# Kernel optimization log

Measured on AMD Instinct MI355X. Metric: run time of the kernel, lower is better.

The kernel has to match this reference:

```python
import jax, jax.numpy as jnp
import numpy as np

B, M, Q, D = 32, 8192, 64, 128

def setup_inputs() -> dict:
    key = jax.random.key(0)
    k1, k2, k3, k4 = jax.random.split(key, 4)
    story_a = jax.random.normal(k1, (B, M, D), dtype=jnp.float32)
    u = jax.random.normal(k2, (B, Q, D), dtype=jnp.float32)
    story_c = jax.random.normal(k3, (B, M, D), dtype=jnp.float32)
    H = jax.random.normal(k4, (D, D), dtype=jnp.float32) * (1.0 / np.sqrt(D))
    return {"story_a": story_a, "u": u, "story_c": story_c, "H": H}

def reference(story_a, u, story_c, H):
    # scores: Dot(axes=-1)([story_a, u]) -> (B, M, Q)
    m = jnp.einsum('bmd,bqd->bmq', story_a, u)
    # Keras Softmax() default axis=-1: normalize over Q (faithful to original)
    p = jax.nn.softmax(m, axis=-1)          # (B, M, Q)
    p = jnp.swapaxes(p, 1, 2)                # (B, Q, M)
    # output memory: Dot(axes=(2,1))([p, story_c]) -> (B, Q, D)
    c = jnp.einsum('bqm,bmd->bqd', p, story_c)
    # linear residual: K.dot(u, H) + c
    mapped_u = jnp.einsum('bqd,de->bqe', u, H)
    return c + mapped_u
```

## Files before the change

### kernel.cpp

```cpp
#include <hip/hip_runtime.h>

#define B_ 32
#define M_ 8192
#define Q_ 64
#define D_ 128
#define MT 64
#define LDA 136
#define LDP 72

typedef __attribute__((ext_vector_type(8))) short short8;
typedef __attribute__((ext_vector_type(4))) float floatx4;

__device__ __forceinline__ unsigned pkbf(float a, float b) {
  unsigned ua = __builtin_bit_cast(unsigned, a) + 0x8000u;
  unsigned ub = __builtin_bit_cast(unsigned, b) + 0x8000u;
  return __builtin_amdgcn_perm(ub, ua, 0x07060302u);
}

template <int CTRL>
__device__ __forceinline__ float dppadd(float x) {
  int y = __builtin_amdgcn_update_dpp(0, __builtin_bit_cast(int, x), CTRL, 0xF, 0xF, true);
  return x + __builtin_bit_cast(float, y);
}
__device__ __forceinline__ float rowsum16(float x) {
  x = dppadd<0x128>(x); x = dppadd<0x124>(x);
  x = dppadd<0x122>(x); x = dppadd<0x121>(x);
  return x;
}

__device__ __forceinline__ void barrier_lds() {
  asm volatile("s_waitcnt lgkmcnt(0)\n\ts_barrier" ::: "memory");
}

__global__ __launch_bounds__(256) void pack_u(const float* __restrict__ U,
                                              short8* __restrict__ ufrag) {
  int t = blockIdx.x * 256 + threadIdx.x;
  int lane = t & 63, ks = (t >> 6) & 3, qs = (t >> 8) & 3, b = t >> 10;
  int l15 = lane & 15, quad = (lane >> 4) & 3;
  const float* p = U + ((size_t)b * Q_ + 16 * qs + l15) * D_ + 32 * ks + 8 * quad;
  float4 x = *(const float4*)p;
  float4 y = *(const float4*)(p + 4);
  union { unsigned u[4]; short8 v; } o;
  o.u[0] = pkbf(x.x, x.y); o.u[1] = pkbf(x.z, x.w);
  o.u[2] = pkbf(y.x, y.y); o.u[3] = pkbf(y.z, y.w);
  ufrag[t] = o.v;
}

__global__ __launch_bounds__(256, 4) void memn2n_main(
    const float* __restrict__ A, const float* __restrict__ Cc,
    const short8* __restrict__ ufrag, float* __restrict__ dst,
    int chunks, int use_atomic) {
  __shared__ __align__(16) unsigned short sAP[MT * LDA];
  __shared__ __align__(16) unsigned short sC[MT * LDA];
  unsigned short* const sA = sAP;
  unsigned short* const sP = sAP;

  const int tid  = threadIdx.x;
  const int lane = tid & 63;
  const int w    = tid >> 6;
  const int l15  = lane & 15;
  const int quad = (lane >> 4) & 3;

  const int blk = blockIdx.x;
  const int b   = blk / chunks;
  const int ch  = blk - b * chunks;
  const int Mc  = M_ / chunks;
  const int nT  = Mc / MT;

  const int g = tid & 31;
  const int r = tid >> 5;

  const short8* ufb = ufrag + (size_t)b * 16 * 64 + lane;

  floatx4 acc[2][4];
#pragma unroll
  for (int i = 0; i < 2; ++i)
#pragma unroll
    for (int j = 0; j < 4; ++j) acc[i][j] = (floatx4){0.f, 0.f, 0.f, 0.f};

  const float* Abase = A + ((size_t)b * M_ + (size_t)ch * Mc) * D_;
  const float* Cbase = Cc + ((size_t)b * M_ + (size_t)ch * Mc) * D_;

  for (int t = 0; t < nT; ++t) {
    const float* At = Abase + (size_t)t * MT * D_;
    const float* Ct = Cbase + (size_t)t * MT * D_;
    barrier_lds();
#pragma unroll
    for (int i = 0; i < 8; ++i) {
      int mi = r + 8 * i;
      float4 v = *(const float4*)(At + mi * D_ + 4 * g);
      *(uint2*)&sA[mi * LDA + 4 * g] = make_uint2(pkbf(v.x, v.y), pkbf(v.z, v.w));
    }
#pragma unroll
    for (int i = 0; i < 8; ++i) {
      int mi = r + 8 * i;
      float4 v = *(const float4*)(Ct + mi * D_ + 4 * g);
      *(uint2*)&sC[mi * LDA + 4 * g] = make_uint2(pkbf(v.x, v.y), pkbf(v.z, v.w));
    }
    barrier_lds();

    floatx4 s1[4];
#pragma unroll
    for (int qs = 0; qs < 4; ++qs) s1[qs] = (floatx4){0.f, 0.f, 0.f, 0.f};
#pragma unroll
    for (int ks = 0; ks < 4; ++ks) {
      short8 af = *(const short8*)&sA[(16 * w + l15) * LDA + 32 * ks + 8 * quad];
#pragma unroll
      for (int qs = 0; qs < 4; ++qs) {
        short8 bfv = ufb[(qs * 4 + ks) * 64];
        s1[qs] = __builtin_amdgcn_mfma_f32_16x16x32_bf16(af, bfv, s1[qs], 0, 0, 0);
      }
    }
    barrier_lds();

    float pv[4][4];
#pragma unroll
    for (int rg = 0; rg < 4; ++rg) {
      const float c = 1.4426950408889634f;
      float e0 = exp2f(s1[0][rg] * c), e1 = exp2f(s1[1][rg] * c);
      float e2 = exp2f(s1[2][rg] * c), e3 = exp2f(s1[3][rg] * c);
      float sm = (e0 + e1) + (e2 + e3);
      sm = rowsum16(sm);
      float inv = __builtin_amdgcn_rcpf(sm);
      pv[0][rg] = e0 * inv; pv[1][rg] = e1 * inv;
      pv[2][rg] = e2 * inv; pv[3][rg] = e3 * inv;
    }
#pragma unroll
    for (int qs = 0; qs < 4; ++qs) {
      *(uint2*)&sP[(16 * qs + l15) * LDP + 16 * w + 4 * quad] =
          make_uint2(pkbf(pv[qs][0], pv[qs][1]), pkbf(pv[qs][2], pv[qs][3]));
    }
    barrier_lds();

#pragma unroll
    for (int ks = 0; ks < 2; ++ks) {
      short8 pa[4];
#pragma unroll
      for (int qs = 0; qs < 4; ++qs)
        pa[qs] = *(const short8*)&sP[(16 * qs + l15) * LDP + 32 * ks + 8 * quad];
#pragma unroll
      for (int ds = 0; ds < 2; ++ds) {
        int d = l15 + 16 * (2 * w + ds);
        union { unsigned short u[8]; short8 v; } bb;
#pragma unroll
        for (int j = 0; j < 8; ++j)
          bb.u[j] = sC[(32 * ks + 8 * quad + j) * LDA + d];
#pragma unroll
        for (int qs = 0; qs < 4; ++qs)
          acc[ds][qs] = __builtin_amdgcn_mfma_f32_16x16x32_bf16(pa[qs], bb.v, acc[ds][qs], 0, 0, 0);
      }
    }
  }

  if (use_atomic) {
#pragma unroll
    for (int ds = 0; ds < 2; ++ds)
#pragma unroll
      for (int qs = 0; qs < 4; ++qs)
#pragma unroll
        for (int rg = 0; rg < 4; ++rg) {
          int q = qs * 16 + quad * 4 + rg;
          int d = l15 + 16 * (2 * w + ds);
          atomicAdd(&dst[((size_t)b * Q_ + q) * D_ + d], acc[ds][qs][rg]);
        }
  } else {
    float* pp = dst + (((size_t)ch * B_ + b) * Q_) * D_;
#pragma unroll
    for (int ds = 0; ds < 2; ++ds)
#pragma unroll
      for (int qs = 0; qs < 4; ++qs)
#pragma unroll
        for (int rg = 0; rg < 4; ++rg) {
          int q = qs * 16 + quad * 4 + rg;
          int d = l15 + 16 * (2 * w + ds);
          pp[q * D_ + d] = acc[ds][qs][rg];
        }
  }
}

__global__ __launch_bounds__(128) void memn2n_reduce(
    const float* __restrict__ U, const float* __restrict__ H,
    const float* __restrict__ part, float* __restrict__ out, int chunks) {
  int bq = blockIdx.x;
  int b = bq >> 6, q = bq & 63;
  int d = threadIdx.x;
  __shared__ float su[D_];
  size_t row = ((size_t)b * Q_ + q) * D_;
  su[d] = U[row + d];
  __syncthreads();
  float acc = 0.f;
#pragma unroll 16
  for (int e = 0; e < D_; ++e) acc = fmaf(su[e], H[e * D_ + d], acc);
#pragma unroll 8
  for (int ch = 0; ch < chunks; ++ch)
    acc += part[(((size_t)ch * B_ + b) * Q_ + q) * D_ + d];
  out[row + d] = acc;
}

extern "C" void kernel_launch(void* const* d_in, const int* in_sizes, int n_in,
                              void* d_out, int out_size, void* d_ws, size_t ws_size,
                              hipStream_t stream) {
  const float* A  = (const float*)d_in[0];
  const float* U  = (const float*)d_in[1];
  const float* Cc = (const float*)d_in[2];
  const float* H  = (const float*)d_in[3];
  float* out = (float*)d_out;

  const size_t upack_bytes = (size_t)B_ * 16 * 64 * 16;

  int CHn = 32;
  size_t part_bytes = (size_t)CHn * B_ * Q_ * D_ * sizeof(float);
  if (ws_size >= part_bytes + upack_bytes) {
    float* part = (float*)d_ws;
    short8* upk = (short8*)((char*)d_ws + part_bytes);
    pack_u<<<128, 256, 0, stream>>>(U, upk);
    memn2n_main<<<B_ * CHn, 256, 0, stream>>>(A, Cc, upk, part, CHn, 0);
    memn2n_reduce<<<B_ * Q_, 128, 0, stream>>>(U, H, part, out, CHn);
    return;
  }
  CHn = 16;
  part_bytes = (size_t)CHn * B_ * Q_ * D_ * sizeof(float);
  if (ws_size >= part_bytes + upack_bytes) {
    float* part = (float*)d_ws;
    short8* upk = (short8*)((char*)d_ws + part_bytes);
    pack_u<<<128, 256, 0, stream>>>(U, upk);
    memn2n_main<<<B_ * CHn, 256, 0, stream>>>(A, Cc, upk, part, CHn, 0);
    memn2n_reduce<<<B_ * Q_, 128, 0, stream>>>(U, H, part, out, CHn);
    return;
  }
  {
    short8* upk = (short8*)d_ws;
    pack_u<<<128, 256, 0, stream>>>(U, upk);
    memn2n_reduce<<<B_ * Q_, 128, 0, stream>>>(U, H, nullptr, out, 0);
    memn2n_main<<<B_ * 8, 256, 0, stream>>>(A, Cc, upk, out, 8, 1);
  }
}
```

Baseline: 309.4 us.

## Double-buffer C tiles via async global-to-LDS DMA and load A straight to registers

Rewrites the main loop to prefetch the next tile. story_c is brought in fp32 through global_load_lds DMA into double-buffered shared memory, and story_a goes straight into registers, so both loads overlap the current tile's compute. Conversion to bf16 now happens after the reads from LDS, U fragments are packed in-kernel (dropping the pack_u launch), and chunks per batch drop from 32 to 16 with unrolled templated tile counts. In exchange the kernel uses more LDS and registers (occupancy hint lowered to 2 blocks per CU) and does bf16 packing on the read side.

Result: faster. 297.1 us (-4.0%).

```diff
diff --git a/kernel.cpp b/kernel.cpp
--- a/kernel.cpp
+++ b/kernel.cpp
@@ -5,8 +5,8 @@
 #define Q_ 64
 #define D_ 128
 #define MT 64
-#define LDA 136
 #define LDP 72
+#define LDCP 260
 
 typedef __attribute__((ext_vector_type(8))) short short8;
 typedef __attribute__((ext_vector_type(4))) float floatx4;
@@ -17,6 +17,13 @@
   return __builtin_amdgcn_perm(ub, ua, 0x07060302u);
 }
 
+__device__ __forceinline__ short8 pack8(float4 a, float4 b) {
+  union { unsigned u[4]; short8 v; } o;
+  o.u[0] = pkbf(a.x, a.y); o.u[1] = pkbf(a.z, a.w);
+  o.u[2] = pkbf(b.x, b.y); o.u[3] = pkbf(b.z, b.w);
+  return o.v;
+}
+
 template <int CTRL>
 __device__ __forceinline__ float dppadd(float x) {
   int y = __builtin_amdgcn_update_dpp(0, __builtin_bit_cast(int, x), CTRL, 0xF, 0xF, true);
@@ -32,28 +39,18 @@
   asm volatile("s_waitcnt lgkmcnt(0)\n\ts_barrier" ::: "memory");
 }
 
-__global__ __launch_bounds__(256) void pack_u(const float* __restrict__ U,
-                                              short8* __restrict__ ufrag) {
-  int t = blockIdx.x * 256 + threadIdx.x;
-  int lane = t & 63, ks = (t >> 6) & 3, qs = (t >> 8) & 3, b = t >> 10;
-  int l15 = lane & 15, quad = (lane >> 4) & 3;
-  const float* p = U + ((size_t)b * Q_ + 16 * qs + l15) * D_ + 32 * ks + 8 * quad;
-  float4 x = *(const float4*)p;
-  float4 y = *(const float4*)(p + 4);
-  union { unsigned u[4]; short8 v; } o;
-  o.u[0] = pkbf(x.x, x.y); o.u[1] = pkbf(x.z, x.w);
-  o.u[2] = pkbf(y.x, y.y); o.u[3] = pkbf(y.z, y.w);
-  ufrag[t] = o.v;
-}
-
-__global__ __launch_bounds__(256, 4) void memn2n_main(
-    const float* __restrict__ A, const float* __restrict__ Cc,
-    const short8* __restrict__ ufrag, float* __restrict__ dst,
-    int chunks, int use_atomic) {
-  __shared__ __align__(16) unsigned short sAP[MT * LDA];
-  __shared__ __align__(16) unsigned short sC[MT * LDA];
-  unsigned short* const sA = sAP;
-  unsigned short* const sP = sAP;
+__device__ __forceinline__ void dma16(const float* g, float* l) {
+  __builtin_amdgcn_global_load_lds(
+      (const __attribute__((address_space(1))) void*)g,
+      (__attribute__((address_space(3))) void*)l, 16, 0, 0);
+}
+
+template <int NT, bool ATOMIC>
+__global__ __launch_bounds__(256, 2) void memn2n_main(
+    const float* __restrict__ A, const float* __restrict__ U,
+    const float* __restrict__ Cc, float* __restrict__ dst) {
+  __shared__ __align__(16) float sCb[2][32 * LDCP];
+  __shared__ __align__(16) unsigned short sP[Q_ * LDP];
 
   const int tid  = threadIdx.x;
   const int lane = tid & 63;
@@ -61,16 +58,46 @@
   const int l15  = lane & 15;
   const int quad = (lane >> 4) & 3;
 
+  constexpr int chunks = (M_ / MT) / NT;
   const int blk = blockIdx.x;
   const int b   = blk / chunks;
   const int ch  = blk - b * chunks;
-  const int Mc  = M_ / chunks;
-  const int nT  = Mc / MT;
-
-  const int g = tid & 31;
-  const int r = tid >> 5;
-
-  const short8* ufb = ufrag + (size_t)b * 16 * 64 + lane;
+
+  const float* Abase = A + ((size_t)b * M_ + (size_t)ch * NT * MT) * D_;
+  const float* Cbase = Cc + ((size_t)b * M_ + (size_t)ch * NT * MT) * D_;
+
+  const float* ub = U + (size_t)b * Q_ * D_;
+  short8 uf[4][4];
+#pragma unroll
+  for (int qs = 0; qs < 4; ++qs)
+#pragma unroll
+    for (int ks = 0; ks < 4; ++ks) {
+      const float* p = ub + (16 * qs + l15) * D_ + 32 * ks + 8 * quad;
+      uf[qs][ks] = pack8(*(const float4*)p, *(const float4*)(p + 4));
+    }
+
+  float4 pA[2][8];
+
+#define DMA_TILE(tt, bi)                                                        \
+  {                                                                             \
+    const float* Ct_ = Cbase + (size_t)(tt) * MT * D_;                          \
+    _Pragma("unroll") for (int j = 0; j < 8; ++j) {                             \
+      int p = w * 8 + j;                                                        \
+      dma16(Ct_ + p * 256 + (lane >> 5) * 128 + (lane & 31) * 4,                \
+            &sCb[bi][p * LDCP]);                                                \
+    }                                                                           \
+  }
+#define LOAD_A(tt, bi)                                                          \
+  {                                                                             \
+    const float* Ar_ = Abase + (size_t)(tt) * MT * D_ + (16 * w + l15) * D_ + 8 * quad; \
+    _Pragma("unroll") for (int ks = 0; ks < 4; ++ks) {                          \
+      pA[bi][2 * ks]     = *(const float4*)(Ar_ + 32 * ks);                     \
+      pA[bi][2 * ks + 1] = *(const float4*)(Ar_ + 32 * ks + 4);                 \
+    }                                                                           \
+  }
+
+  DMA_TILE(0, 0);
+  LOAD_A(0, 0);
 
   floatx4 acc[2][4];
 #pragma unroll
@@ -78,40 +105,20 @@
 #pragma unroll
     for (int j = 0; j < 4; ++j) acc[i][j] = (floatx4){0.f, 0.f, 0.f, 0.f};
 
-  const float* Abase = A + ((size_t)b * M_ + (size_t)ch * Mc) * D_;
-  const float* Cbase = Cc + ((size_t)b * M_ + (size_t)ch * Mc) * D_;
-
-  for (int t = 0; t < nT; ++t) {
-    const float* At = Abase + (size_t)t * MT * D_;
-    const float* Ct = Cbase + (size_t)t * MT * D_;
-    barrier_lds();
-#pragma unroll
-    for (int i = 0; i < 8; ++i) {
-      int mi = r + 8 * i;
-      float4 v = *(const float4*)(At + mi * D_ + 4 * g);
-      *(uint2*)&sA[mi * LDA + 4 * g] = make_uint2(pkbf(v.x, v.y), pkbf(v.z, v.w));
-    }
-#pragma unroll
-    for (int i = 0; i < 8; ++i) {
-      int mi = r + 8 * i;
-      float4 v = *(const float4*)(Ct + mi * D_ + 4 * g);
-      *(uint2*)&sC[mi * LDA + 4 * g] = make_uint2(pkbf(v.x, v.y), pkbf(v.z, v.w));
-    }
-    barrier_lds();
+#pragma unroll
+  for (int t = 0; t < NT; ++t) {
+    const int cur = t & 1, nxt = cur ^ 1;
 
     floatx4 s1[4];
 #pragma unroll
     for (int qs = 0; qs < 4; ++qs) s1[qs] = (floatx4){0.f, 0.f, 0.f, 0.f};
 #pragma unroll
     for (int ks = 0; ks < 4; ++ks) {
-      short8 af = *(const short8*)&sA[(16 * w + l15) * LDA + 32 * ks + 8 * quad];
-#pragma unroll
-      for (int qs = 0; qs < 4; ++qs) {
-        short8 bfv = ufb[(qs * 4 + ks) * 64];
-        s1[qs] = __builtin_amdgcn_mfma_f32_16x16x32_bf16(af, bfv, s1[qs], 0, 0, 0);
-      }
-    }
-    barrier_lds();
+      short8 af = pack8(pA[cur][2 * ks], pA[cur][2 * ks + 1]);
+#pragma unroll
+      for (int qs = 0; qs < 4; ++qs)
+        s1[qs] = __builtin_amdgcn_mfma_f32_16x16x32_bf16(af, uf[qs][ks], s1[qs], 0, 0, 0);
+    }
 
     float pv[4][4];
 #pragma unroll
@@ -125,11 +132,19 @@
       pv[0][rg] = e0 * inv; pv[1][rg] = e1 * inv;
       pv[2][rg] = e2 * inv; pv[3][rg] = e3 * inv;
     }
-#pragma unroll
-    for (int qs = 0; qs < 4; ++qs) {
+
+    barrier_lds();
+
+    if (t + 1 < NT) {
+      DMA_TILE(t + 1, nxt);
+      LOAD_A(t + 1, nxt);
+    }
+
+#pragma unroll
+    for (int qs = 0; qs < 4; ++qs)
       *(uint2*)&sP[(16 * qs + l15) * LDP + 16 * w + 4 * quad] =
           make_uint2(pkbf(pv[qs][0], pv[qs][1]), pkbf(pv[qs][2], pv[qs][3]));
-    }
+
     barrier_lds();
 
 #pragma unroll
@@ -141,18 +156,21 @@
 #pragma unroll
       for (int ds = 0; ds < 2; ++ds) {
         int d = l15 + 16 * (2 * w + ds);
-        union { unsigned short u[8]; short8 v; } bb;
+        float cc[8];
 #pragma unroll
         for (int j = 0; j < 8; ++j)
-          bb.u[j] = sC[(32 * ks + 8 * quad + j) * LDA + d];
+          cc[j] = sCb[cur][(16 * ks + 4 * quad + (j >> 1)) * LDCP + (j & 1) * 128 + d];
+        union { unsigned u[4]; short8 v; } o;
+        o.u[0] = pkbf(cc[0], cc[1]); o.u[1] = pkbf(cc[2], cc[3]);
+        o.u[2] = pkbf(cc[4], cc[5]); o.u[3] = pkbf(cc[6], cc[7]);
 #pragma unroll
         for (int qs = 0; qs < 4; ++qs)
-          acc[ds][qs] = __builtin_amdgcn_mfma_f32_16x16x32_bf16(pa[qs], bb.v, acc[ds][qs], 0, 0, 0);
+          acc[ds][qs] = __builtin_amdgcn_mfma_f32_16x16x32_bf16(pa[qs], o.v, acc[ds][qs], 0, 0, 0);
       }
     }
   }
 
-  if (use_atomic) {
+  if (ATOMIC) {
 #pragma unroll
     for (int ds = 0; ds < 2; ++ds)
 #pragma unroll
@@ -176,6 +194,8 @@
           pp[q * D_ + d] = acc[ds][qs][rg];
         }
   }
+#undef DMA_TILE
+#undef LOAD_A
 }
 
 __global__ __launch_bounds__(128) void memn2n_reduce(
@@ -206,32 +226,14 @@
   const float* H  = (const float*)d_in[3];
   float* out = (float*)d_out;
 
-  const size_t upack_bytes = (size_t)B_ * 16 * 64 * 16;
-
-  int CHn = 32;
+  const int CHn = 16;
   size_t part_bytes = (size_t)CHn * B_ * Q_ * D_ * sizeof(float);
-  if (ws_size >= part_bytes + upack_bytes) {
+  if (ws_size >= part_bytes) {
     float* part = (float*)d_ws;
-    short8* upk = (short8*)((char*)d_ws + part_bytes);
-    pack_u<<<128, 256, 0, stream>>>(U, upk);
-    memn2n_main<<<B_ * CHn, 256, 0, stream>>>(A, Cc, upk, part, CHn, 0);
+    memn2n_main<8, false><<<B_ * CHn, 256, 0, stream>>>(A, U, Cc, part);
     memn2n_reduce<<<B_ * Q_, 128, 0, stream>>>(U, H, part, out, CHn);
-    return;
-  }
-  CHn = 16;
-  part_bytes = (size_t)CHn * B_ * Q_ * D_ * sizeof(float);
-  if (ws_size >= part_bytes + upack_bytes) {
-    float* part = (float*)d_ws;
-    short8* upk = (short8*)((char*)d_ws + part_bytes);
-    pack_u<<<128, 256, 0, stream>>>(U, upk);
-    memn2n_main<<<B_ * CHn, 256, 0, stream>>>(A, Cc, upk, part, CHn, 0);
-    memn2n_reduce<<<B_ * Q_, 128, 0, stream>>>(U, H, part, out, CHn);
-    return;
-  }
-  {
-    short8* upk = (short8*)d_ws;
-    pack_u<<<128, 256, 0, stream>>>(U, upk);
+  } else {
     memn2n_reduce<<<B_ * Q_, 128, 0, stream>>>(U, H, nullptr, out, 0);
-    memn2n_main<<<B_ * 8, 256, 0, stream>>>(A, Cc, upk, out, 8, 1);
-  }
-}
+    memn2n_main<16, true><<<B_ * 8, 256, 0, stream>>>(A, U, Cc, out);
+  }
+}
```
